# Kernel optimization log

Hardware: AMD Instinct MI355X
Metric: run time of the kernel (lower is better)

## Reference

```python
import jax, jax.numpy as jnp
import numpy as np

E, N, LAT = 200000, 50000, 128
EPS = 1e-8

def _split(x):
    # irreps layout 64x0e | 32x1e | 16x2e, mul-major: [E,64], [E,32,3], [E,16,5]
    n = x.shape[0]
    return x[:, :64], x[:, 64:160].reshape(n, 32, 3), x[:, 160:240].reshape(n, 16, 5)

def _merge(x0, x1, x2):
    n = x0.shape[0]
    return jnp.concatenate([x0, x1.reshape(n, -1), x2.reshape(n, -1)], axis=-1)

def _sep_ln(x, w0, b0, w1, w2):
    # separable layer norm: standard LN on l=0 scalars, degree-balanced RMS on l>0
    x0, x1, x2 = _split(x)
    x0c = x0 - x0.mean(-1, keepdims=True)
    y0 = x0c * jax.lax.rsqrt((x0c * x0c).mean(-1, keepdims=True) + EPS) * w0 + b0
    var = 0.5 * ((x1 * x1).mean((-2, -1)) + (x2 * x2).mean((-2, -1)))
    inv = jax.lax.rsqrt(var + EPS)[:, None, None]
    return _merge(y0, x1 * inv * w1[None, :, None], x2 * inv * w2[None, :, None])

def _rot(x0, x1, x2, D, back=False):
    # per-l Wigner-D block rotation; D is block-diag [E,9,9] (l=0:1x1, l=1:3x3, l=2:5x5)
    sub = 'eji,ecj->eci' if back else 'eij,ecj->eci'
    y0 = x0 * D[:, 0, 0][:, None]
    y1 = jnp.einsum(sub, D[:, 1:4, 1:4], x1)
    y2 = jnp.einsum(sub, D[:, 4:9, 4:9], x2)
    return y0, y1, y2

def _silu(x):
    return x * jax.nn.sigmoid(x)

def _forward(latents, node_features, edge_features, edge_vector, wigner_D_all,
             ln_n_w0, ln_n_b0, ln_n_w1, ln_n_w2, ln_e_w0, ln_e_b0, ln_e_w1, ln_e_w2,
             so2_w0, so2_w1r, so2_w1i, so2_w2r, so2_w2i, lp_w0, lp_b0, lp_w1, lp_w2,
             edge_index, active_edges):
    nn = _sep_ln(node_features, ln_n_w0, ln_n_b0, ln_n_w1, ln_n_w2)
    ne = _sep_ln(edge_features, ln_e_w0, ln_e_b0, ln_e_w1, ln_e_w2)
    ec = edge_index[0][active_edges]
    en = edge_index[1][active_edges]
    lat = latents[active_edges]
    D = wigner_D_all
    # rotate each segment (center | edge | neighbor) into the edge frame (tp_rotate_in)
    segs = [_rot(*_split(s), D) for s in (nn[ec], ne, nn[en])]
    # group by SO(2) order m (index within (2l+1) components is l+m)
    m0 = jnp.concatenate([jnp.concatenate([s0, s1[:, :, 1], s2[:, :, 2]], -1) for s0, s1, s2 in segs] + [lat], -1)  # [E,464]
    p1 = jnp.concatenate([jnp.concatenate([s1[:, :, 2], s2[:, :, 3]], -1) for _, s1, s2 in segs], -1)  # [E,144]
    n1 = jnp.concatenate([jnp.concatenate([s1[:, :, 0], s2[:, :, 1]], -1) for _, s1, s2 in segs], -1)
    p2 = jnp.concatenate([s2[:, :, 4] for _, _, s2 in segs], -1)  # [E,48]
    n2 = jnp.concatenate([s2[:, :, 0] for _, _, s2 in segs], -1)
    # SO(2) linear: real map for m=0 (latents injected), complex 2x2 maps for m>0
    o0 = (m0 @ so2_w0) * (1.0 / np.sqrt(464.0))  # [E,160] = 112 scalars+gates | 32 l1-m0 | 16 l2-m0
    inv1 = 1.0 / np.sqrt(144.0)
    op1 = (p1 @ so2_w1r - n1 @ so2_w1i) * inv1
    on1 = (p1 @ so2_w1i + n1 @ so2_w1r) * inv1
    inv2 = 1.0 / np.sqrt(48.0)
    op2 = (p2 @ so2_w2r - n2 @ so2_w2i) * inv2
    on2 = (p2 @ so2_w2i + n2 @ so2_w2r) * inv2
    s0 = o0[:, :112]
    o1 = jnp.stack([on1[:, :32], o0[:, 112:144], op1[:, :32]], -1)              # [E,32,3]
    o2 = jnp.stack([on2, on1[:, 32:], o0[:, 144:160], op1[:, 32:], op2], -1)   # [E,16,5]
    # rotate back out of the edge frame (tp_rotate_out)
    s0, o1, o2 = _rot(s0, o1, o2, D, back=True)
    # Gate: silu on 64 scalars, sigmoid gates (48) multiply l>0 channels
    gates = jax.nn.sigmoid(s0[:, 64:112])
    sc = _silu(s0[:, :64])
    g1 = o1 * gates[:, :32, None]
    g2 = o2 * gates[:, 32:, None]
    # lin_post: per-l channel-mixing linear, bias on scalars only
    y0 = sc @ lp_w0 * (1.0 / np.sqrt(64.0)) + lp_b0
    y1 = jnp.einsum('ecm,cd->edm', g1, lp_w1) * (1.0 / np.sqrt(32.0))
    y2 = jnp.einsum('ecm,cd->edm', g2, lp_w2) * (1.0 / np.sqrt(16.0))
    return _merge(y0, y1, y2)  # [E,240]

def setup_inputs() -> dict:
    key = jax.random.key(0)
    k = lambda i: jax.random.fold_in(key, i)
    f = lambda i, sh: jax.random.normal(k(i), sh, dtype=jnp.float32)
    return dict(
        latents=f(0, (E, LAT)),
        node_features=f(1, (N, 240)),
        edge_features=f(2, (E, 240)),
        edge_vector=f(3, (E, 3)),
        wigner_D_all=f(4, (E, 9, 9)),
        ln_n_w0=f(5, (64,)), ln_n_b0=f(6, (64,)) * 0.1, ln_n_w1=f(7, (32,)), ln_n_w2=f(8, (16,)),
        ln_e_w0=f(9, (64,)), ln_e_b0=f(10, (64,)) * 0.1, ln_e_w1=f(11, (32,)), ln_e_w2=f(12, (16,)),
        so2_w0=f(13, (464, 160)), so2_w1r=f(14, (144, 48)), so2_w1i=f(15, (144, 48)),
        so2_w2r=f(16, (48, 16)), so2_w2i=f(17, (48, 16)),
        lp_w0=f(18, (64, 64)), lp_b0=f(19, (64,)) * 0.1, lp_w1=f(20, (32, 32)), lp_w2=f(21, (16, 16)),
        edge_index=jax.random.randint(k(22), (2, E), 0, N, dtype=jnp.int32),
        active_edges=jnp.arange(E, dtype=jnp.int32),
    )

def reference(latents, node_features, edge_features, edge_vector, wigner_D_all,
              ln_n_w0, ln_n_b0, ln_n_w1, ln_n_w2, ln_e_w0, ln_e_b0, ln_e_w1, ln_e_w2,
              so2_w0, so2_w1r, so2_w1i, so2_w2r, so2_w2i, lp_w0, lp_b0, lp_w1, lp_w2,
              edge_index, active_edges):
    return _forward(latents, node_features, edge_features, edge_vector, wigner_D_all,
                    ln_n_w0, ln_n_b0, ln_n_w1, ln_n_w2, ln_e_w0, ln_e_b0, ln_e_w1, ln_e_w2,
                    so2_w0, so2_w1r, so2_w1i, so2_w2r, so2_w2i, lp_w0, lp_b0, lp_w1, lp_w2,
                    edge_index, active_edges)
```

## Files before the change

kernel.cpp:

```cpp
#include <hip/hip_runtime.h>
#include <hip/hip_bf16.h>
#include <math.h>

#define NT 256
#define EB 16

using sv4    = __attribute__((ext_vector_type(4))) short;
using short8 = __attribute__((ext_vector_type(8))) short;
using f32x4  = __attribute__((ext_vector_type(4))) float;
using f32x2  = __attribute__((ext_vector_type(2))) float;
typedef unsigned short u16;
typedef unsigned int   u32;

#define MFMA(a,b,c) __builtin_amdgcn_mfma_f32_16x16x32_bf16((a),(b),(c),0,0,0)

#define FW0   0
#define FW1R  150
#define FW1I  165
#define FW1IN 180
#define FW2R  195
#define FW2I  197
#define FW2IN 199
#define FL0   201
#define FL1   209
#define FL2   211
#define NFRAG 212
#define WS_NLS_OFF (NFRAG * 512)

__device__ __forceinline__ u16 f2b(float x) {
  union { float f; u32 u; } v; v.f = x;
  return (u16)((v.u + 0x8000u) >> 16);
}
__device__ __forceinline__ float b2f(u16 u) {
  union { float f; u32 u; } v; v.u = ((u32)u) << 16;
  return v.f;
}
__device__ __forceinline__ sv4 ld4(const u16* p){ return *reinterpret_cast<const sv4*>(p); }

__global__ void prep_w(const float* __restrict__ w0,
                       const float* __restrict__ w1r, const float* __restrict__ w1i,
                       const float* __restrict__ w2r, const float* __restrict__ w2i,
                       const float* __restrict__ l0,  const float* __restrict__ l1,
                       const float* __restrict__ l2,  u16* __restrict__ ws) {
  const int g = blockIdx.x * 256 + threadIdx.x;
  if (g >= NFRAG * 64) return;
  const int frag = g >> 6, lane = g & 63;
  const float* src; int K, N, kt, nt; float sgn = 1.f;
  if (frag < FW1R)       { src = w0;  K = 464; N = 160; int f = frag;       kt = f/10; nt = f%10; }
  else if (frag < FW1I)  { src = w1r; K = 144; N = 48;  int f = frag-FW1R;  kt = f/3;  nt = f%3; }
  else if (frag < FW1IN) { src = w1i; K = 144; N = 48;  int f = frag-FW1I;  kt = f/3;  nt = f%3; }
  else if (frag < FW2R)  { src = w1i; K = 144; N = 48;  int f = frag-FW1IN; kt = f/3;  nt = f%3; sgn = -1.f; }
  else if (frag < FW2I)  { src = w2r; K = 48;  N = 16;  kt = frag-FW2R; nt = 0; }
  else if (frag < FW2IN) { src = w2i; K = 48;  N = 16;  kt = frag-FW2I; nt = 0; }
  else if (frag < FL0)   { src = w2i; K = 48;  N = 16;  kt = frag-FW2IN; nt = 0; sgn = -1.f; }
  else if (frag < FL1)   { src = l0;  K = 64;  N = 64;  int f = frag-FL0;   kt = f/4;  nt = f%4; }
  else if (frag < FL2)   { src = l1;  K = 32;  N = 32;  kt = 0; nt = frag-FL1; }
  else                   { src = l2;  K = 16;  N = 16;  kt = 0; nt = 0; }
  const int n  = nt*16 + (lane & 15);
  const int k0 = kt*32 + (lane >> 4) * 8;
  u16* dst = ws + (size_t)frag * 512 + lane * 8;
  #pragma unroll
  for (int j = 0; j < 8; ++j) {
    const int k = k0 + j;
    const float v = (k < K && n < N) ? src[k * N + n] * sgn : 0.f;
    dst[j] = f2b(v);
  }
}

__global__ void ln_nodes(const float* __restrict__ nodef,
                         const float* __restrict__ w0, const float* __restrict__ b0,
                         const float* __restrict__ w1, const float* __restrict__ w2,
                         u16* __restrict__ nls, int N) {
  const int row  = blockIdx.x * 4 + (threadIdx.x >> 6);
  const int lane = threadIdx.x & 63;
  if (row >= N) return;
  const float* src = nodef + (size_t)row * 240;
  const float v0 = src[lane];
  const float v1 = src[lane + 64];
  const float v2 = src[lane + 128];
  const float v3 = (lane < 48) ? src[lane + 192] : 0.f;
  const bool lo = (lane < 32);
  float sm = v0, sq = v0*v0;
  float S1 = v1*v1 + (lo ? v2*v2 : 0.f);
  float S2 = (lo ? 0.f : v2*v2) + v3*v3;
  #pragma unroll
  for (int s = 32; s > 0; s >>= 1) {
    sm += __shfl_xor(sm, s, 64); sq += __shfl_xor(sq, s, 64);
    S1 += __shfl_xor(S1, s, 64); S2 += __shfl_xor(S2, s, 64);
  }
  const float mu  = sm * (1.f/64.f);
  const float i0  = rsqrtf(sq*(1.f/64.f) - mu*mu + 1e-8f);
  const float inv = rsqrtf(0.5f*(S1*(1.f/96.f) + S2*(1.f/80.f)) + 1e-8f);
  u16* dst = nls + (size_t)row * 320;
  dst[lane] = f2b((v0 - mu) * i0 * w0[lane] + b0[lane]);
  { const int u = lane;      const int c = u/3, j = u-3*c; dst[64 + 4*c + j]  = f2b(v1*inv*w1[c]); }
  if (lo) { const int u = lane+64; const int c = u/3, j = u-3*c; dst[64 + 4*c + j]  = f2b(v2*inv*w1[c]); }
  else    { const int u = lane-32; const int c = u/5, j = u-5*c; dst[192 + 8*c + j] = f2b(v2*inv*w2[c]); }
  if (lane < 48) { const int u = lane+32; const int c = u/5, j = u-5*c; dst[192 + 8*c + j] = f2b(v3*inv*w2[c]); }
  if (lane < 32) dst[64 + 4*lane + 3] = 0;
  if (lane < 48) { const int c = lane/3, j = lane-3*c; dst[192 + 8*c + 5 + j] = 0; }
}

__global__ __launch_bounds__(NT, 4)
void iel_mfma(const float* __restrict__ latents,
              const float* __restrict__ edgef,
              const float* __restrict__ wig,
              const float* __restrict__ ln_e_w0, const float* __restrict__ ln_e_b0,
              const float* __restrict__ ln_e_w1, const float* __restrict__ ln_e_w2,
              const float* __restrict__ lp_b0,
              const int* __restrict__ edge_index, const int* __restrict__ active_edges,
              const u16* __restrict__ ws, const u16* __restrict__ nls,
              float* __restrict__ out,
              int Etot, int A)
{
  __shared__ __align__(16) char SMEM[39072];
  u16*   m0   = (u16*)(SMEM);
  u16*   p1   = (u16*)(SMEM + 15120);
  u16*   n1   = (u16*)(SMEM + 20000);
  u16*   p2   = (u16*)(SMEM + 24880);
  u16*   n2   = (u16*)(SMEM + 26688);
  float* scr  = (float*)(SMEM + 28496);
  float* Dc   = (float*)(SMEM + 32336);
  u16*   g2s  = (u16*)(SMEM + 35152);
  float* o0f  = (float*)(SMEM);
  u16*   g1s  = (u16*)(SMEM + 11008);
  float* op1f = (float*)(SMEM + 15120);
  float* on1f = (float*)(SMEM + 20000);
  float* op2f = (float*)(SMEM + 24880);
  float* on2f = (float*)(SMEM + 26688);
  u16*   gates= (u16*)(SMEM + 28496);
  u16*   scs  = (u16*)(SMEM + 30032);
  float* ot   = (float*)(SMEM + 15120);

  const short8* WF = (const short8*)ws;
  const int t    = threadIdx.x;
  const int lane = t & 63;
  const int w    = t >> 6;
  const int eb0  = blockIdx.x * EB;
  const f32x4 Z4 = {0.f, 0.f, 0.f, 0.f};

  {
    const int r = t >> 4, c = t & 15;
    if (c < 8) {
      m0[r*472 + 464 + c] = 0;
      p1[r*152 + 144 + c] = 0;
      n1[r*152 + 144 + c] = 0;
      p2[r*56  + 48  + c] = 0;
      n2[r*56  + 48  + c] = 0;
      #pragma unroll
      for (int m = 0; m < 5; ++m) g2s[m*392 + r*24 + 16 + c] = 0;
    }
    if (t < 8) {
      m0[16*472 + t] = 0;
      p1[16*152 + t] = 0;
      n1[16*152 + t] = 0;
      p2[16*56  + t] = 0;
      n2[16*56  + t] = 0;
      #pragma unroll
      for (int m = 0; m < 5; ++m) g2s[m*392 + 384 + t] = 0;
    }
  }

  const int cls = (lane < 32) ? 0 : ((lane < 48) ? 1 : 2);
  const int cc  = (cls == 0) ? lane : (lane & 15);
  const int dbase = (cls == 0) ? 1 : ((cls == 1) ? 12 : 27);
  const int dstr  = (cls == 0) ? 3 : 5;

  const int c1 = lane / 3;
  const bool q2lo = (lane < 32);
  const int c2 = q2lo ? (lane + 64) / 3 : (lane - 32) / 5;
  const int c3 = (lane < 48) ? (lane + 32) / 5 : 15;
  const float w0e = ln_e_w0[lane], b0e = ln_e_b0[lane];
  const float wAe = ln_e_w1[c1];
  const float wBe = q2lo ? ln_e_w1[c2] : ln_e_w2[c2];
  const float wCe = ln_e_w2[c3];

  float* swr = scr + w * 240;

  int aev[4], ecv[4], env[4];
  #pragma unroll
  for (int it = 0; it < 4; ++it) {
    const int e = eb0 + (w<<2) + it;
    aev[it] = active_edges[(e < A) ? e : (A-1)];
  }
  #pragma unroll
  for (int it = 0; it < 4; ++it) {
    ecv[it] = edge_index[aev[it]];
    env[it] = edge_index[Etot + aev[it]];
  }

  #pragma unroll
  for (int it = 0; it < 4; ++it) {
    const int el = (w<<2) + it;
    const int e  = eb0 + el;
    const int eS = (e < A) ? e : (A-1);
    if (lane < 35) {
      int src, dst;
      if (lane == 0)      { src = 0; dst = 0; }
      else if (lane < 10) { const int a=(lane-1)/3, b=(lane-1)-3*((lane-1)/3); src=(1+a)*9+(1+b); dst=lane; }
      else                { const int a=(lane-10)/5, b=(lane-10)-5*((lane-10)/5); src=(4+a)*9+(4+b); dst=lane+2; }
      Dc[el*44 + dst] = wig[(size_t)eS*81 + src];
    } else if (lane < 44) {
      const int dst = (lane == 35) ? 10 : (lane == 36) ? 11 : lane;
      Dc[el*44 + dst] = 0.f;
    }
  }

  struct ER {
    u16 q0a, q0b, x4a, x4b;
    sv4 xa, xb;
    float e0, e1, e2, e3, l0, l1;
  };
  ER RA, RB;
  const int xoff = (cls == 0) ? (64 + 4*lane) : (192 + 8*cc);

  auto issue = [&](int it, ER& R) {
    const int e  = eb0 + (w<<2) + it;
    const int eS = (e < A) ? e : (A-1);
    const u16* nba = nls + (size_t)ecv[it]*320;
    const u16* nbb = nls + (size_t)env[it]*320;
    R.q0a = nba[lane]; R.q0b = nbb[lane];
    R.xa = ld4(nba + xoff); R.xb = ld4(nbb + xoff);
    R.x4a = (cls == 0) ? (u16)0 : nba[xoff + 4];
    R.x4b = (cls == 0) ? (u16)0 : nbb[xoff + 4];
    const float* ep = edgef + (size_t)eS*240;
    R.e0 = ep[lane]; R.e1 = ep[lane+64]; R.e2 = ep[lane+128];
    R.e3 = (lane < 48) ? ep[lane+192] : 0.f;
    const float* lr = latents + (size_t)aev[it]*128;
    R.l0 = lr[lane]; R.l1 = lr[64+lane];
  };

  auto process = [&](int it, ER& R) {
    const int el = (w<<2) + it;
    const float* DcE = Dc + el*44;
    const float d00 = DcE[0];
    float d[3][5];
    #pragma unroll
    for (int i = 0; i < 3; ++i)
      #pragma unroll
      for (int j = 0; j < 5; ++j)
        d[i][j] = DcE[dbase + i*dstr + j];

    u16* B0; u16* B1; u16* B2; int S0, S1, S2;
    if (cls == 0)      { B0 = n1 + el*152 + cc;      S0 = 48;  B1 = m0 + el*472 + 64 + cc; S1 = 112; B2 = p1 + el*152 + cc;      S2 = 48; }
    else if (cls == 1) { B0 = n2 + el*56  + cc;      S0 = 16;  B1 = n1 + el*152 + 32 + cc; S1 = 48;  B2 = m0 + el*472 + 96 + cc; S2 = 112; }
    else               { B0 = p1 + el*152 + 32 + cc; S0 = 48;  B1 = p2 + el*56  + cc;      S1 = 16;  B2 = m0;                    S2 = 0; }

    {
      f32x2 x0 = {b2f((u16)R.xa[0]), b2f((u16)R.xb[0])};
      f32x2 x1 = {b2f((u16)R.xa[1]), b2f((u16)R.xb[1])};
      f32x2 x2 = {b2f((u16)R.xa[2]), b2f((u16)R.xb[2])};
      f32x2 x3 = {b2f((u16)R.xa[3]), b2f((u16)R.xb[3])};
      f32x2 x4 = {b2f(R.x4a), b2f(R.x4b)};
      f32x2 q0 = {b2f(R.q0a), b2f(R.q0b)};
      f32x2 q0d = q0 * d00;
      m0[el*472 + lane]       = f2b(q0d[0]);
      m0[el*472 + 224 + lane] = f2b(q0d[1]);
      f32x2 s0 = x0*d[0][0] + x1*d[0][1] + x2*d[0][2] + x3*d[0][3] + x4*d[0][4];
      f32x2 s1 = x0*d[1][0] + x1*d[1][1] + x2*d[1][2] + x3*d[1][3] + x4*d[1][4];
      f32x2 s2 = x0*d[2][0] + x1*d[2][1] + x2*d[2][2] + x3*d[2][3] + x4*d[2][4];
      B0[0] = f2b(s0[0]); B0[2*S0] = f2b(s0[1]);
      B1[0] = f2b(s1[0]); B1[2*S1] = f2b(s1[1]);
      if (lane < 48) { B2[0] = f2b(s2[0]); B2[2*S2] = f2b(s2[1]); }
    }

    {
      const float v0 = R.e0, v1 = R.e1, v2 = R.e2, v3 = R.e3;
      float sm = v0, sq = v0*v0;
      float S1r = v1*v1 + (q2lo ? v2*v2 : 0.f);
      float S2r = (q2lo ? 0.f : v2*v2) + v3*v3;
      #pragma unroll
      for (int s = 32; s > 0; s >>= 1) {
        sm += __shfl_xor(sm, s, 64);  sq += __shfl_xor(sq, s, 64);
        S1r += __shfl_xor(S1r, s, 64); S2r += __shfl_xor(S2r, s, 64);
      }
      const float mu = sm * (1.f/64.f);
      const float i0 = rsqrtf(sq*(1.f/64.f) - mu*mu + 1e-8f);
      const float iv = rsqrtf(0.5f*(S1r*(1.f/96.f) + S2r*(1.f/80.f)) + 1e-8f);
      swr[lane]      = v1 * iv * wAe;
      swr[64 + lane] = v2 * iv * wBe;
      if (lane < 48) swr[128 + lane] = v3 * iv * wCe;
      asm volatile("s_waitcnt lgkmcnt(0)" ::: "memory");
      m0[el*472 + 112 + lane] = f2b(((v0 - mu)*i0*w0e + b0e) * d00);
      const float* sb = (cls == 0) ? (swr + 3*cc) : (swr + 96 + 5*cc);
      const float x0 = sb[0], x1 = sb[1], x2 = sb[2];
      const float x3 = (cls == 0) ? 0.f : sb[3];
      const float x4 = (cls == 0) ? 0.f : sb[4];
      float s0v = d[0][0]*x0 + d[0][1]*x1 + d[0][2]*x2 + d[0][3]*x3 + d[0][4]*x4;
      float s1v = d[1][0]*x0 + d[1][1]*x1 + d[1][2]*x2 + d[1][3]*x3 + d[1][4]*x4;
      float s2v = d[2][0]*x0 + d[2][1]*x1 + d[2][2]*x2 + d[2][3]*x3 + d[2][4]*x4;
      B0[S0] = f2b(s0v);
      B1[S1] = f2b(s1v);
      if (lane < 48) B2[S2] = f2b(s2v);
    }
    m0[el*472 + 336 + lane] = f2b(R.l0);
    m0[el*472 + 400 + lane] = f2b(R.l1);
  };

  issue(0, RA);
  issue(1, RB); process(0, RA);
  issue(2, RA); process(1, RB);
  issue(3, RB); process(2, RA);
  process(3, RB);
  __syncthreads();

  f32x4 acc2a[3] = {Z4, Z4, Z4};
  {
    const u16* abase = m0 + (lane & 15)*472 + (lane >> 4)*8;
    #pragma unroll
    for (int kt = 0; kt < 15; ++kt) {
      const short8 a = *reinterpret_cast<const short8*>(abase + kt*32);
      #pragma unroll
      for (int i = 0; i < 3; ++i) {
        const int nt = w + 4*i;
        if (nt < 10)
          acc2a[i] = MFMA(a, WF[(size_t)(FW0 + kt*10 + nt)*64 + lane], acc2a[i]);
      }
    }
  }
  f32x4 acc2b[2] = {Z4, Z4};
  f32x4 acc2c = Z4;
  {
    const u16* pbase = p1 + (lane & 15)*152 + (lane >> 4)*8;
    const u16* nbase = n1 + (lane & 15)*152 + (lane >> 4)*8;
    #pragma unroll
    for (int kt = 0; kt < 5; ++kt) {
      const short8 pa = *reinterpret_cast<const short8*>(pbase + kt*32);
      const short8 na = *reinterpret_cast<const short8*>(nbase + kt*32);
      #pragma unroll
      for (int i = 0; i < 2; ++i) {
        const int tau = w + 4*i;
        if (tau < 6) {
          const int isOn = (tau >= 3) ? 1 : 0;
          const int nt2 = tau - 3*isOn;
          acc2b[i] = MFMA(pa, WF[(size_t)((isOn?FW1I:FW1R)  + kt*3 + nt2)*64 + lane], acc2b[i]);
          acc2b[i] = MFMA(na, WF[(size_t)((isOn?FW1R:FW1IN) + kt*3 + nt2)*64 + lane], acc2b[i]);
        }
      }
    }
    if (w >= 2) {
      const u16* pb2 = p2 + (lane & 15)*56 + (lane >> 4)*8;
      const u16* nb2 = n2 + (lane & 15)*56 + (lane >> 4)*8;
      const int isOn2 = (w == 3);
      #pragma unroll
      for (int kt = 0; kt < 2; ++kt) {
        const short8 pa = *reinterpret_cast<const short8*>(pb2 + kt*32);
        const short8 na = *reinterpret_cast<const short8*>(nb2 + kt*32);
        acc2c = MFMA(pa, WF[(size_t)((isOn2?FW2I:FW2R)  + kt)*64 + lane], acc2c);
        acc2c = MFMA(na, WF[(size_t)((isOn2?FW2R:FW2IN) + kt)*64 + lane], acc2c);
      }
    }
  }
  __syncthreads();

  {
    #pragma unroll
    for (int i = 0; i < 3; ++i) {
      const int nt = w + 4*i;
      if (nt < 10) {
        const int col = nt*16 + (lane & 15);
        const int r0  = (lane >> 4)*4;
        #pragma unroll
        for (int j = 0; j < 4; ++j)
          o0f[(r0+j)*172 + col] = acc2a[i][j] * 0.046423835f;
      }
    }
  }
  __syncthreads();

  {
    #pragma unroll
    for (int i = 0; i < 2; ++i) {
      const int tau = w + 4*i;
      if (tau < 6) {
        const int isOn = (tau >= 3) ? 1 : 0;
        const int nt2 = tau - 3*isOn;
        float* dst = isOn ? on1f : op1f;
        const int col = nt2*16 + (lane & 15);
        const int r0  = (lane >> 4)*4;
        #pragma unroll
        for (int j = 0; j < 4; ++j)
          dst[(r0+j)*52 + col] = acc2b[i][j] * (1.f/12.f);
      }
    }
    if (w >= 2) {
      float* dst = (w == 3) ? on2f : op2f;
      const int r0 = (lane >> 4)*4;
      #pragma unroll
      for (int j = 0; j < 4; ++j)
        dst[(r0+j)*20 + (lane & 15)] = acc2c[j] * 0.14433757f;
    }
  }
  {
    const int e = t >> 4, l16 = t & 15;
    const float d0 = Dc[e*44];
    #pragma unroll
    for (int k = 0; k < 7; ++k) {
      const int p = l16 + 16*k;
      const float x = o0f[e*172 + p] * d0;
      const float sg = 1.f/(1.f + __expf(-x));
      if (p < 64) scs[e*72 + p] = f2b(x * sg);
      else        gates[e*48 + (p - 64)] = f2b(sg);
    }
  }
  __syncthreads();

  {
    const int e = t >> 4, l16 = t & 15;
    const float* DcE = Dc + e*44;
    #pragma unroll
    for (int k = 0; k < 6; ++k) {
      const int item = l16 + 16*k;
      const int c = item/3, m = item - 3*c;
      const float val = DcE[1 + m]     * on1f[e*52 + c]
                      + DcE[1 + 3 + m] * o0f[e*172 + 112 + c]
                      + DcE[1 + 6 + m] * op1f[e*52 + c];
      const float g = b2f(gates[e*48 + c]);
      g1s[m*640 + e*40 + c] = f2b(val * g);
    }
    const int c = l16;
    const float f0 = on2f[e*20 + c];
    const float f1 = on1f[e*52 + 32 + c];
    const float f2c = o0f[e*172 + 144 + c];
    const float f3 = op1f[e*52 + 32 + c];
    const float f4 = op2f[e*20 + c];
    const float gg = b2f(gates[e*48 + 32 + c]);
    #pragma unroll
    for (int m = 0; m < 5; ++m) {
      const float val = DcE[12 + m]*f0 + DcE[12 + 5 + m]*f1 + DcE[12 + 10 + m]*f2c
                      + DcE[12 + 15 + m]*f3 + DcE[12 + 20 + m]*f4;
      g2s[m*392 + e*24 + c] = f2b(val * gg);
    }
  }
  __syncthreads();

  for (int tau = w; tau < 15; tau += 4) {
    const int col16 = lane & 15;
    const int r0 = (lane >> 4)*4;
    if (tau < 4) {
      const int ntt = tau;
      f32x4 a0 = Z4;
      #pragma unroll
      for (int kt = 0; kt < 2; ++kt) {
        const short8 a = *reinterpret_cast<const short8*>(
            scs + (lane & 15)*72 + kt*32 + (lane >> 4)*8);
        a0 = MFMA(a, WF[(size_t)(FL0 + kt*4 + ntt)*64 + lane], a0);
      }
      const int col = ntt*16 + col16;
      const float bias = lp_b0[col];
      #pragma unroll
      for (int j = 0; j < 4; ++j) {
        const int er = eb0 + r0 + j;
        if (er < A) out[(size_t)er*240 + col] = a0[j]*0.125f + bias;
      }
    } else if (tau < 10) {
      const int u = tau - 4, m = u >> 1, ntt = u & 1;
      const short8 a = *reinterpret_cast<const short8*>(
          g1s + m*640 + (lane & 15)*40 + (lane >> 4)*8);
      f32x4 a0 = Z4;
      a0 = MFMA(a, WF[(size_t)(FL1 + ntt)*64 + lane], a0);
      const int oc = (ntt*16 + col16)*3 + m;
      #pragma unroll
      for (int j = 0; j < 4; ++j)
        ot[(r0+j)*176 + oc] = a0[j]*0.17677670f;
    } else {
      const int m = tau - 10;
      const short8 a = *reinterpret_cast<const short8*>(
          g2s + m*392 + (lane & 15)*24 + (lane >> 4)*8);
      f32x4 a0 = Z4;
      a0 = MFMA(a, WF[(size_t)FL2*64 + lane], a0);
      const int oc = 96 + col16*5 + m;
      #pragma unroll
      for (int j = 0; j < 4; ++j)
        ot[(r0+j)*176 + oc] = a0[j]*0.25f;
    }
  }
  __syncthreads();

  for (int idx = t; idx < 16*44; idx += NT) {
    const int row = idx / 44, seg = idx - row*44;
    const int er = eb0 + row;
    if (er < A) {
      const f32x4 v = *reinterpret_cast<const f32x4*>(ot + row*176 + seg*4);
      *reinterpret_cast<f32x4*>(out + (size_t)er*240 + 64 + seg*4) = v;
    }
  }
}

extern "C" void kernel_launch(void* const* d_in, const int* in_sizes, int n_in,
                              void* d_out, int out_size, void* d_ws, size_t ws_size,
                              hipStream_t stream) {
  const float* latents  = (const float*)d_in[0];
  const float* nodef    = (const float*)d_in[1];
  const float* edgef    = (const float*)d_in[2];
  const float* wig      = (const float*)d_in[4];
  const float* ln_n_w0  = (const float*)d_in[5];
  const float* ln_n_b0  = (const float*)d_in[6];
  const float* ln_n_w1  = (const float*)d_in[7];
  const float* ln_n_w2  = (const float*)d_in[8];
  const float* ln_e_w0  = (const float*)d_in[9];
  const float* ln_e_b0  = (const float*)d_in[10];
  const float* ln_e_w1  = (const float*)d_in[11];
  const float* ln_e_w2  = (const float*)d_in[12];
  const float* so2_w0   = (const float*)d_in[13];
  const float* so2_w1r  = (const float*)d_in[14];
  const float* so2_w1i  = (const float*)d_in[15];
  const float* so2_w2r  = (const float*)d_in[16];
  const float* so2_w2i  = (const float*)d_in[17];
  const float* lp_w0    = (const float*)d_in[18];
  const float* lp_b0    = (const float*)d_in[19];
  const float* lp_w1    = (const float*)d_in[20];
  const float* lp_w2    = (const float*)d_in[21];
  const int*   edge_index   = (const int*)d_in[22];
  const int*   active_edges = (const int*)d_in[23];

  const int Etot = in_sizes[2] / 240;
  const int N    = in_sizes[1] / 240;
  const int A    = in_sizes[23];

  u16* ws  = (u16*)d_ws;
  u16* nls = ws + WS_NLS_OFF;

  const int pthreads = NFRAG * 64;
  hipLaunchKernelGGL(prep_w, dim3((pthreads + 255) / 256), dim3(256), 0, stream,
                     so2_w0, so2_w1r, so2_w1i, so2_w2r, so2_w2i,
                     lp_w0, lp_w1, lp_w2, ws);

  hipLaunchKernelGGL(ln_nodes, dim3((N + 3) / 4), dim3(256), 0, stream,
                     nodef, ln_n_w0, ln_n_b0, ln_n_w1, ln_n_w2, nls, N);

  const int grid = (A + EB - 1) / EB;
  hipLaunchKernelGGL(iel_mfma, dim3(grid), dim3(NT), 0, stream,
                     latents, edgef, wig,
                     ln_e_w0, ln_e_b0, ln_e_w1, ln_e_w2,
                     lp_b0, edge_index, active_edges, ws, nls,
                     (float*)d_out, Etot, A);
}
```

Before: 407.2 us.

## Double threads per block to eight waves and redistribute per-edge and MFMA work

Raises the block size from 256 to 512 threads, so each wave preprocesses two edges instead of four and the MFMA output tiles are split across eight waves. Shared memory is rearranged: the Dc stride shrinks from 44 to 40 and g2s is moved, so its zeroing is deferred until after the scratch region is no longer needed. The goal is more parallelism and latency hiding per block of 16 edges. The cost is tighter register limits at eight waves, idle waves in the smaller GEMM phases, and less software pipelining of the gather loads.

Result: slower. 430.1 us (+5.6%).

```diff
diff --git a/kernel.cpp b/kernel.cpp
--- a/kernel.cpp
+++ b/kernel.cpp
@@ -2,7 +2,7 @@
 #include <hip/hip_bf16.h>
 #include <math.h>
 
-#define NT 256
+#define NT 512
 #define EB 16
 
 using sv4    = __attribute__((ext_vector_type(4))) short;
@@ -101,7 +101,7 @@
   if (lane < 48) { const int c = lane/3, j = lane-3*c; dst[192 + 8*c + 5 + j] = 0; }
 }
 
-__global__ __launch_bounds__(NT, 4)
+__global__ __launch_bounds__(NT, 8)
 void iel_mfma(const float* __restrict__ latents,
               const float* __restrict__ edgef,
               const float* __restrict__ wig,
@@ -113,15 +113,15 @@
               float* __restrict__ out,
               int Etot, int A)
 {
-  __shared__ __align__(16) char SMEM[39072];
+  __shared__ __align__(16) char SMEM[38848];
   u16*   m0   = (u16*)(SMEM);
   u16*   p1   = (u16*)(SMEM + 15120);
   u16*   n1   = (u16*)(SMEM + 20000);
   u16*   p2   = (u16*)(SMEM + 24880);
   u16*   n2   = (u16*)(SMEM + 26688);
   float* scr  = (float*)(SMEM + 28496);
-  float* Dc   = (float*)(SMEM + 32336);
-  u16*   g2s  = (u16*)(SMEM + 35152);
+  float* Dc   = (float*)(SMEM + 36256);
+  u16*   g2s  = (u16*)(SMEM + 32336);
   float* o0f  = (float*)(SMEM);
   u16*   g1s  = (u16*)(SMEM + 11008);
   float* op1f = (float*)(SMEM + 15120);
@@ -139,7 +139,7 @@
   const int eb0  = blockIdx.x * EB;
   const f32x4 Z4 = {0.f, 0.f, 0.f, 0.f};
 
-  {
+  if (t < 256) {
     const int r = t >> 4, c = t & 15;
     if (c < 8) {
       m0[r*472 + 464 + c] = 0;
@@ -147,8 +147,6 @@
       n1[r*152 + 144 + c] = 0;
       p2[r*56  + 48  + c] = 0;
       n2[r*56  + 48  + c] = 0;
-      #pragma unroll
-      for (int m = 0; m < 5; ++m) g2s[m*392 + r*24 + 16 + c] = 0;
     }
     if (t < 8) {
       m0[16*472 + t] = 0;
@@ -156,8 +154,6 @@
       n1[16*152 + t] = 0;
       p2[16*56  + t] = 0;
       n2[16*56  + t] = 0;
-      #pragma unroll
-      for (int m = 0; m < 5; ++m) g2s[m*392 + 384 + t] = 0;
     }
   }
 
@@ -175,23 +171,23 @@
   const float wBe = q2lo ? ln_e_w1[c2] : ln_e_w2[c2];
   const float wCe = ln_e_w2[c3];
 
-  float* swr = scr + w * 240;
-
-  int aev[4], ecv[4], env[4];
+  float* swr = scr + w * 176;
+
+  int aev[2], ecv[2], env[2];
   #pragma unroll
-  for (int it = 0; it < 4; ++it) {
-    const int e = eb0 + (w<<2) + it;
+  for (int it = 0; it < 2; ++it) {
+    const int e = eb0 + (w<<1) + it;
     aev[it] = active_edges[(e < A) ? e : (A-1)];
   }
   #pragma unroll
-  for (int it = 0; it < 4; ++it) {
+  for (int it = 0; it < 2; ++it) {
     ecv[it] = edge_index[aev[it]];
     env[it] = edge_index[Etot + aev[it]];
   }
 
   #pragma unroll
-  for (int it = 0; it < 4; ++it) {
-    const int el = (w<<2) + it;
+  for (int it = 0; it < 2; ++it) {
+    const int el = (w<<1) + it;
     const int e  = eb0 + el;
     const int eS = (e < A) ? e : (A-1);
     if (lane < 35) {
@@ -199,10 +195,9 @@
       if (lane == 0)      { src = 0; dst = 0; }
       else if (lane < 10) { const int a=(lane-1)/3, b=(lane-1)-3*((lane-1)/3); src=(1+a)*9+(1+b); dst=lane; }
       else                { const int a=(lane-10)/5, b=(lane-10)-5*((lane-10)/5); src=(4+a)*9+(4+b); dst=lane+2; }
-      Dc[el*44 + dst] = wig[(size_t)eS*81 + src];
-    } else if (lane < 44) {
-      const int dst = (lane == 35) ? 10 : (lane == 36) ? 11 : lane;
-      Dc[el*44 + dst] = 0.f;
+      Dc[el*40 + dst] = wig[(size_t)eS*81 + src];
+    } else if (lane < 37) {
+      Dc[el*40 + (lane - 25)] = 0.f;
     }
   }
 
@@ -215,7 +210,7 @@
   const int xoff = (cls == 0) ? (64 + 4*lane) : (192 + 8*cc);
 
   auto issue = [&](int it, ER& R) {
-    const int e  = eb0 + (w<<2) + it;
+    const int e  = eb0 + (w<<1) + it;
     const int eS = (e < A) ? e : (A-1);
     const u16* nba = nls + (size_t)ecv[it]*320;
     const u16* nbb = nls + (size_t)env[it]*320;
@@ -231,8 +226,8 @@
   };
 
   auto process = [&](int it, ER& R) {
-    const int el = (w<<2) + it;
-    const float* DcE = Dc + el*44;
+    const int el = (w<<1) + it;
+    const float* DcE = Dc + el*40;
     const float d00 = DcE[0];
     float d[3][5];
     #pragma unroll
@@ -298,93 +293,77 @@
   };
 
   issue(0, RA);
-  issue(1, RB); process(0, RA);
-  issue(2, RA); process(1, RB);
-  issue(3, RB); process(2, RA);
-  process(3, RB);
+  issue(1, RB);
+  process(0, RA);
+  process(1, RB);
   __syncthreads();
 
-  f32x4 acc2a[3] = {Z4, Z4, Z4};
+  f32x4 acc2a[2] = {Z4, Z4};
   {
     const u16* abase = m0 + (lane & 15)*472 + (lane >> 4)*8;
     #pragma unroll
     for (int kt = 0; kt < 15; ++kt) {
       const short8 a = *reinterpret_cast<const short8*>(abase + kt*32);
-      #pragma unroll
-      for (int i = 0; i < 3; ++i) {
-        const int nt = w + 4*i;
-        if (nt < 10)
-          acc2a[i] = MFMA(a, WF[(size_t)(FW0 + kt*10 + nt)*64 + lane], acc2a[i]);
-      }
-    }
-  }
-  f32x4 acc2b[2] = {Z4, Z4};
+      acc2a[0] = MFMA(a, WF[(size_t)(FW0 + kt*10 + w)*64 + lane], acc2a[0]);
+      if (w < 2)
+        acc2a[1] = MFMA(a, WF[(size_t)(FW0 + kt*10 + 8 + w)*64 + lane], acc2a[1]);
+    }
+  }
+  f32x4 acc2b = Z4;
   f32x4 acc2c = Z4;
-  {
+  if (w < 6) {
     const u16* pbase = p1 + (lane & 15)*152 + (lane >> 4)*8;
     const u16* nbase = n1 + (lane & 15)*152 + (lane >> 4)*8;
+    const int isOn = (w >= 3) ? 1 : 0;
+    const int nt2 = w - 3*isOn;
     #pragma unroll
     for (int kt = 0; kt < 5; ++kt) {
       const short8 pa = *reinterpret_cast<const short8*>(pbase + kt*32);
       const short8 na = *reinterpret_cast<const short8*>(nbase + kt*32);
-      #pragma unroll
-      for (int i = 0; i < 2; ++i) {
-        const int tau = w + 4*i;
-        if (tau < 6) {
-          const int isOn = (tau >= 3) ? 1 : 0;
-          const int nt2 = tau - 3*isOn;
-          acc2b[i] = MFMA(pa, WF[(size_t)((isOn?FW1I:FW1R)  + kt*3 + nt2)*64 + lane], acc2b[i]);
-          acc2b[i] = MFMA(na, WF[(size_t)((isOn?FW1R:FW1IN) + kt*3 + nt2)*64 + lane], acc2b[i]);
-        }
-      }
-    }
-    if (w >= 2) {
-      const u16* pb2 = p2 + (lane & 15)*56 + (lane >> 4)*8;
-      const u16* nb2 = n2 + (lane & 15)*56 + (lane >> 4)*8;
-      const int isOn2 = (w == 3);
-      #pragma unroll
-      for (int kt = 0; kt < 2; ++kt) {
-        const short8 pa = *reinterpret_cast<const short8*>(pb2 + kt*32);
-        const short8 na = *reinterpret_cast<const short8*>(nb2 + kt*32);
-        acc2c = MFMA(pa, WF[(size_t)((isOn2?FW2I:FW2R)  + kt)*64 + lane], acc2c);
-        acc2c = MFMA(na, WF[(size_t)((isOn2?FW2R:FW2IN) + kt)*64 + lane], acc2c);
-      }
+      acc2b = MFMA(pa, WF[(size_t)((isOn?FW1I:FW1R)  + kt*3 + nt2)*64 + lane], acc2b);
+      acc2b = MFMA(na, WF[(size_t)((isOn?FW1R:FW1IN) + kt*3 + nt2)*64 + lane], acc2b);
+    }
+  } else {
+    const u16* pb2 = p2 + (lane & 15)*56 + (lane >> 4)*8;
+    const u16* nb2 = n2 + (lane & 15)*56 + (lane >> 4)*8;
+    const int isOn2 = (w == 7);
+    #pragma unroll
+    for (int kt = 0; kt < 2; ++kt) {
+      const short8 pa = *reinterpret_cast<const short8*>(pb2 + kt*32);
+      const short8 na = *reinterpret_cast<const short8*>(nb2 + kt*32);
+      acc2c = MFMA(pa, WF[(size_t)((isOn2?FW2I:FW2R)  + kt)*64 + lane], acc2c);
+      acc2c = MFMA(na, WF[(size_t)((isOn2?FW2R:FW2IN) + kt)*64 + lane], acc2c);
     }
   }
   __syncthreads();
 
   {
-    #pragma unroll
-    for (int i = 0; i < 3; ++i) {
-      const int nt = w + 4*i;
-      if (nt < 10) {
-        const int col = nt*16 + (lane & 15);
-        const int r0  = (lane >> 4)*4;
-        #pragma unroll
-        for (int j = 0; j < 4; ++j)
-          o0f[(r0+j)*172 + col] = acc2a[i][j] * 0.046423835f;
-      }
+    const int col = w*16 + (lane & 15);
+    const int r0  = (lane >> 4)*4;
+    #pragma unroll
+    for (int j = 0; j < 4; ++j)
+      o0f[(r0+j)*172 + col] = acc2a[0][j] * 0.046423835f;
+    if (w < 2) {
+      const int col2 = (8+w)*16 + (lane & 15);
+      #pragma unroll
+      for (int j = 0; j < 4; ++j)
+        o0f[(r0+j)*172 + col2] = acc2a[1][j] * 0.046423835f;
     }
   }
   __syncthreads();
 
   {
-    #pragma unroll
-    for (int i = 0; i < 2; ++i) {
-      const int tau = w + 4*i;
-      if (tau < 6) {
-        const int isOn = (tau >= 3) ? 1 : 0;
-        const int nt2 = tau - 3*isOn;
-        float* dst = isOn ? on1f : op1f;
-        const int col = nt2*16 + (lane & 15);
-        const int r0  = (lane >> 4)*4;
-        #pragma unroll
-        for (int j = 0; j < 4; ++j)
-          dst[(r0+j)*52 + col] = acc2b[i][j] * (1.f/12.f);
-      }
-    }
-    if (w >= 2) {
-      float* dst = (w == 3) ? on2f : op2f;
+    if (w < 6) {
+      const int isOn = (w >= 3) ? 1 : 0;
+      const int nt2 = w - 3*isOn;
+      float* dst = isOn ? on1f : op1f;
+      const int col = nt2*16 + (lane & 15);
+      const int r0  = (lane >> 4)*4;
+      #pragma unroll
+      for (int j = 0; j < 4; ++j)
+        dst[(r0+j)*52 + col] = acc2b[j] * (1.f/12.f);
+    } else {
+      float* dst = (w == 7) ? on2f : op2f;
       const int r0 = (lane >> 4)*4;
       #pragma unroll
       for (int j = 0; j < 4; ++j)
@@ -392,25 +371,38 @@
     }
   }
   {
-    const int e = t >> 4, l16 = t & 15;
-    const float d0 = Dc[e*44];
-    #pragma unroll
-    for (int k = 0; k < 7; ++k) {
-      const int p = l16 + 16*k;
-      const float x = o0f[e*172 + p] * d0;
-      const float sg = 1.f/(1.f + __expf(-x));
-      if (p < 64) scs[e*72 + p] = f2b(x * sg);
-      else        gates[e*48 + (p - 64)] = f2b(sg);
+    const int e = t >> 5, l32 = t & 31;
+    const float d0 = Dc[e*40];
+    #pragma unroll
+    for (int k = 0; k < 4; ++k) {
+      const int p = l32 + 32*k;
+      if (p < 112) {
+        const float x = o0f[e*172 + p] * d0;
+        const float sg = 1.f/(1.f + __expf(-x));
+        if (p < 64) scs[e*72 + p] = f2b(x * sg);
+        else        gates[e*48 + (p - 64)] = f2b(sg);
+      }
+    }
+  }
+  if (t < 256) {
+    const int r = t >> 4, c = t & 15;
+    if (c < 8) {
+      #pragma unroll
+      for (int m = 0; m < 5; ++m) g2s[m*392 + r*24 + 16 + c] = 0;
+    }
+    if (t < 8) {
+      #pragma unroll
+      for (int m = 0; m < 5; ++m) g2s[m*392 + 384 + t] = 0;
     }
   }
   __syncthreads();
 
   {
-    const int e = t >> 4, l16 = t & 15;
-    const float* DcE = Dc + e*44;
-    #pragma unroll
-    for (int k = 0; k < 6; ++k) {
-      const int item = l16 + 16*k;
+    const int e = t >> 5, l32 = t & 31;
+    const float* DcE = Dc + e*40;
+    #pragma unroll
+    for (int k = 0; k < 3; ++k) {
+      const int item = l32 + 32*k;
       const int c = item/3, m = item - 3*c;
       const float val = DcE[1 + m]     * on1f[e*52 + c]
                       + DcE[1 + 3 + m] * o0f[e*172 + 112 + c]
@@ -418,23 +410,25 @@
       const float g = b2f(gates[e*48 + c]);
       g1s[m*640 + e*40 + c] = f2b(val * g);
     }
-    const int c = l16;
-    const float f0 = on2f[e*20 + c];
-    const float f1 = on1f[e*52 + 32 + c];
-    const float f2c = o0f[e*172 + 144 + c];
-    const float f3 = op1f[e*52 + 32 + c];
-    const float f4 = op2f[e*20 + c];
-    const float gg = b2f(gates[e*48 + 32 + c]);
-    #pragma unroll
-    for (int m = 0; m < 5; ++m) {
-      const float val = DcE[12 + m]*f0 + DcE[12 + 5 + m]*f1 + DcE[12 + 10 + m]*f2c
-                      + DcE[12 + 15 + m]*f3 + DcE[12 + 20 + m]*f4;
-      g2s[m*392 + e*24 + c] = f2b(val * gg);
+    if (l32 < 16) {
+      const int c = l32;
+      const float f0 = on2f[e*20 + c];
+      const float f1 = on1f[e*52 + 32 + c];
+      const float f2c = o0f[e*172 + 144 + c];
+      const float f3 = op1f[e*52 + 32 + c];
+      const float f4 = op2f[e*20 + c];
+      const float gg = b2f(gates[e*48 + 32 + c]);
+      #pragma unroll
+      for (int m = 0; m < 5; ++m) {
+        const float val = DcE[12 + m]*f0 + DcE[12 + 5 + m]*f1 + DcE[12 + 10 + m]*f2c
+                        + DcE[12 + 15 + m]*f3 + DcE[12 + 20 + m]*f4;
+        g2s[m*392 + e*24 + c] = f2b(val * gg);
+      }
     }
   }
   __syncthreads();
 
-  for (int tau = w; tau < 15; tau += 4) {
+  for (int tau = w; tau < 15; tau += 8) {
     const int col16 = lane & 15;
     const int r0 = (lane >> 4)*4;
     if (tau < 4) {
```
